# Kernel optimization log

Measured on AMD Instinct MI355X. Metric: run time of the kernel, lower is better.

Reference implementation:

```python
import jax, jax.numpy as jnp
import numpy as np

B, CIN, COUT, N, T, K = 16, 32, 64, 1024, 64, 3


def setup_inputs() -> dict:
    key = jax.random.key(0)
    k1, k2, k3 = jax.random.split(key, 3)
    x = jax.random.normal(k1, (B, CIN, N, T), dtype=jnp.float32)
    # scaled laplacian-like support (keep spectral radius ~1 so Chebyshev terms stay bounded)
    adj = jax.random.normal(k2, (N, N), dtype=jnp.float32) / np.sqrt(N).astype(np.float32)
    W = jax.random.normal(k3, (4 * COUT, (CIN + COUT) * K), dtype=jnp.float32) * 0.02
    b = jnp.zeros((4 * COUT,), dtype=jnp.float32)
    return {"x": x, "adj": adj, "W": W, "b": b}


def reference(x, adj, W, b):
    Bn, cin, Nn, Tn = x.shape
    c_out = W.shape[0] // 4
    feat_in = W.shape[1] // K  # = cin + c_out

    # Chebyshev polynomial basis of adj (loop-invariant across time; compute once)
    Ls = [jnp.eye(Nn, dtype=x.dtype), adj]
    for _ in range(2, K):
        Ls.append(2.0 * (adj @ Ls[-1]) - Ls[-2])
    Lap = jnp.stack(Ls, 0)  # [K, N, N]; Ls[k][q, n]

    # Conv1d(kernel=1) weight reshaped to match channel flatten order (c major, k minor)
    Wr = W.reshape(4 * c_out, feat_in, K)  # [4*c_out, F, K]
    bb = b[None, :, None]

    def step(carry, xt):
        h, c = carry
        tem = jnp.concatenate([xt, h], axis=1)  # [B, F, N]
        # einsum('bcn,knq->bckq', x, Lap.T) == einsum('bfn,kqn->bfkq', x, Lap)
        g = jnp.einsum('bfn,kqn->bfkq', tem, Lap)  # [B, F, K, N]
        fea = jnp.einsum('bfkq,ofk->boq', g, Wr) + bb  # [B, 4*c_out, N]
        i, j, f, o = jnp.split(fea, 4, axis=1)
        new_c = c * jax.nn.sigmoid(f) + jax.nn.sigmoid(i) * jnp.tanh(j)
        new_h = jnp.tanh(new_c) * jax.nn.sigmoid(o)
        return (new_h, new_c), new_h

    h0 = jnp.zeros((Bn, c_out, Nn), dtype=x.dtype)
    c0 = jnp.zeros((Bn, c_out, Nn), dtype=x.dtype)
    x_t = jnp.moveaxis(x, -1, 0)  # [T, B, cin, N]
    _, outs = jax.lax.scan(step, (h0, c0), x_t)  # [T, B, c_out, N]
    return jnp.moveaxis(outs, 0, -1)  # [B, c_out, N, T]
```

## Files before the change

kernel.cpp:

```cpp
#include <hip/hip_runtime.h>
#include <stdint.h>


#define Bb   16
#define CIN  32
#define COUT 64
#define Nn   1024
#define Tt   64
#define Ff   96
#define G4   256
#define KJ   288

#define BUFSZ 57344
#define GQLO  37888
#define GQP   592

typedef unsigned short u16;
typedef short short8 __attribute__((ext_vector_type(8)));
typedef short short4v __attribute__((ext_vector_type(4)));
typedef float f32x4 __attribute__((ext_vector_type(4)));

static __device__ __forceinline__ u16 f2bf(float f) {
    union { float f; uint32_t u; } v; v.f = f;
    uint32_t r = v.u + 0x7FFFu + ((v.u >> 16) & 1u);
    return (u16)(r >> 16);
}
static __device__ __forceinline__ float bf2f(u16 h) {
    union { uint32_t u; float f; } v; v.u = ((uint32_t)h) << 16;
    return v.f;
}
static __device__ __forceinline__ float sigm(float x) { return 1.0f / (1.0f + expf(-x)); }

static __device__ __forceinline__ void gload16(const void* g, void* l) {
    __builtin_amdgcn_global_load_lds(
        (const __attribute__((address_space(1))) void*)g,
        (__attribute__((address_space(3))) void*)l, 16, 0, 0);
}

__global__ void k_fill(float* out, int n, float v) {
    int i = blockIdx.x * 256 + threadIdx.x;
    if (i < n) out[i] = v;
}

__global__ __launch_bounds__(256) void k_adj_split(const float* __restrict__ adj,
                                                   u16* __restrict__ hi, u16* __restrict__ lo) {
    int i = blockIdx.x * 256 + threadIdx.x;
    float v = adj[i];
    u16 h = f2bf(v);
    hi[i] = h; lo[i] = f2bf(v - bf2f(h));
}

__global__ __launch_bounds__(256) void k_adj_t(const float* __restrict__ adj,
                                               u16* __restrict__ th, u16* __restrict__ tl_) {
    __shared__ float tile[64][65];
    int m0 = blockIdx.x * 64, n0 = blockIdx.y * 64;
    int tid = threadIdx.x;
    #pragma unroll
    for (int i = 0; i < 16; i++) {
        int lin = i * 256 + tid;
        int ml = lin >> 6, nl = lin & 63;
        tile[ml][nl] = adj[(size_t)(m0 + ml) * Nn + n0 + nl];
    }
    __syncthreads();
    #pragma unroll
    for (int i = 0; i < 16; i++) {
        int lin = i * 256 + tid;
        int nl = lin >> 6, ml = lin & 63;
        float v = tile[ml][nl];
        u16 h = f2bf(v);
        size_t off = (size_t)(n0 + nl) * Nn + m0 + ml;
        th[off] = h; tl_[off] = f2bf(v - bf2f(h));
    }
}

__global__ __launch_bounds__(256) void k_l2(
    const u16* __restrict__ a_hi, const u16* __restrict__ a_lo,
    const u16* __restrict__ bt_hi, const u16* __restrict__ bt_lo,
    u16* __restrict__ o_hi, u16* __restrict__ o_lo)
{
    __shared__ u16 Ah[64][40], Al[64][40], Bh[64][40], Bl[64][40];
    const int tid = threadIdx.x, lane = tid & 63, w = tid >> 6;
    const int wm = (w >> 1) * 32, wn = (w & 1) * 32;
    const int r0 = blockIdx.x * 64, q0 = blockIdx.y * 64;
    const int srow = tid >> 2, scol = (tid & 3) * 8;
    const u16* arh = a_hi + (size_t)(r0 + srow) * Nn;
    const u16* arl = a_lo + (size_t)(r0 + srow) * Nn;
    const u16* brh = bt_hi + (size_t)(q0 + srow) * Nn;
    const u16* brl = bt_lo + (size_t)(q0 + srow) * Nn;

    f32x4 acc[2][2];
    #pragma unroll
    for (int i = 0; i < 2; i++)
        #pragma unroll
        for (int j = 0; j < 2; j++) acc[i][j] = (f32x4){0.f, 0.f, 0.f, 0.f};

    for (int k0 = 0; k0 < Nn; k0 += 32) {
        __syncthreads();
        *(short8*)&Ah[srow][scol] = *(const short8*)&arh[k0 + scol];
        *(short8*)&Al[srow][scol] = *(const short8*)&arl[k0 + scol];
        *(short8*)&Bh[srow][scol] = *(const short8*)&brh[k0 + scol];
        *(short8*)&Bl[srow][scol] = *(const short8*)&brl[k0 + scol];
        __syncthreads();
        const int kb = (lane >> 4) * 8;
        short8 ah[2], al[2], bh[2], bl[2];
        #pragma unroll
        for (int mi = 0; mi < 2; mi++) {
            int row = wm + mi * 16 + (lane & 15);
            ah[mi] = *(const short8*)&Ah[row][kb];
            al[mi] = *(const short8*)&Al[row][kb];
        }
        #pragma unroll
        for (int ni = 0; ni < 2; ni++) {
            int col = wn + ni * 16 + (lane & 15);
            bh[ni] = *(const short8*)&Bh[col][kb];
            bl[ni] = *(const short8*)&Bl[col][kb];
        }
        #pragma unroll
        for (int mi = 0; mi < 2; mi++)
            #pragma unroll
            for (int ni = 0; ni < 2; ni++) {
                acc[mi][ni] = __builtin_amdgcn_mfma_f32_16x16x32_bf16(ah[mi], bh[ni], acc[mi][ni], 0, 0, 0);
                acc[mi][ni] = __builtin_amdgcn_mfma_f32_16x16x32_bf16(al[mi], bh[ni], acc[mi][ni], 0, 0, 0);
                acc[mi][ni] = __builtin_amdgcn_mfma_f32_16x16x32_bf16(ah[mi], bl[ni], acc[mi][ni], 0, 0, 0);
            }
    }
    #pragma unroll
    for (int mi = 0; mi < 2; mi++)
        #pragma unroll
        for (int ni = 0; ni < 2; ni++)
            #pragma unroll
            for (int j = 0; j < 4; j++) {
                int rr = r0 + wm + mi * 16 + (lane >> 4) * 4 + j;
                int qq = q0 + wn + ni * 16 + (lane & 15);
                float v = 2.f * acc[mi][ni][j] - ((rr == qq) ? 1.f : 0.f);
                size_t off = (size_t)rr * Nn + qq;
                u16 hh = f2bf(v);
                o_hi[off] = hh; o_lo[off] = f2bf(v - bf2f(hh));
            }
}

__global__ __launch_bounds__(256) void k_w_split(const float* __restrict__ W,
                                                 u16* __restrict__ hi, u16* __restrict__ lo) {
    int idx = blockIdx.x * 256 + threadIdx.x;
    int o = idx / KJ, j = idx - o * KJ;
    int k = j / Ff, f = j - k * Ff;
    float v = W[(size_t)o * KJ + f * 3 + k];
    u16 h = f2bf(v);
    hi[idx] = h; lo[idx] = f2bf(v - bf2f(h));
}

__global__ __launch_bounds__(256) void k_x_split(const float* __restrict__ x,
        u16* __restrict__ xf_hi, u16* __restrict__ xf_lo,
        u16* __restrict__ xq_hi, u16* __restrict__ xq_lo) {
    __shared__ float tile[64][65];
    int n0 = blockIdx.x * 64;
    int bc = blockIdx.y;
    const float* src = x + (size_t)bc * Nn * Tt;
    int tid = threadIdx.x;
    #pragma unroll
    for (int i = 0; i < 16; i++) {
        int lin = i * 256 + tid;
        int nl = lin >> 6, tl = lin & 63;
        tile[nl][tl] = src[(size_t)(n0 + nl) * Tt + tl];
    }
    __syncthreads();
    int b = bc >> 5, ch = bc & 31;
    #pragma unroll
    for (int i = 0; i < 16; i++) {
        int lin = i * 256 + tid;
        int tl = lin >> 6, nl = lin & 63;
        float v = tile[nl][tl];
        u16 h = f2bf(v), l = f2bf(v - bf2f(h));
        size_t off = (((size_t)tl * Bb + b) * CIN + ch) * Nn + n0 + nl;
        xf_hi[off] = h; xf_lo[off] = l;
        size_t off2 = (((size_t)tl * Bb + b) * Nn + n0 + nl) * CIN + ch;
        xq_hi[off2] = h; xq_lo[off2] = l;
    }
}

__global__ __launch_bounds__(512) void k_step(
    int t,
    const u16* __restrict__ xsf_hi, const u16* __restrict__ xsf_lo,
    const u16* __restrict__ xsq_hi, const u16* __restrict__ xsq_lo,
    u16* __restrict__ hf_hi, u16* __restrict__ hf_lo,
    u16* __restrict__ hq_hi, u16* __restrict__ hq_lo,
    const u16* __restrict__ bcat_hi, const u16* __restrict__ bcat_lo,
    const u16* __restrict__ Wh, const u16* __restrict__ Wl,
    const float* __restrict__ bias, float* __restrict__ cbuf,
    float* __restrict__ outbuf)
{
    __shared__ __attribute__((aligned(16))) char lds[114688];
    const int tid = threadIdx.x, lane = tid & 63, w = tid >> 6;
    const int q0 = blockIdx.x * 64;
    const int bb = blockIdx.y;

    const u16* srcb[7];
    #pragma unroll
    for (int i = 0; i < 7; i++) {
        int u = (i * 8 + w) * 64 + lane;
        if (u < 1536) {
            int hl = (u >= 768) ? 1 : 0;
            int r = (u - hl * 768) >> 3, c8 = u & 7;
            const u16* p;
            if (r < CIN) p = (hl ? xsf_lo : xsf_hi) + (size_t)((t * Bb + bb) * CIN + r) * Nn;
            else         p = (hl ? hf_lo  : hf_hi ) + (size_t)(bb * COUT + r - CIN) * Nn;
            srcb[i] = p + (c8 ^ (r & 7)) * 8;
        } else {
            int v = u - 1536;
            int hl = v >> 10;
            int r = (v & 1023) >> 3, c8 = v & 7;
            int grow = q0 + r + ((r >= 64) ? (Nn - 64) : 0);
            srcb[i] = (hl ? bcat_lo : bcat_hi) + (size_t)grow * Nn + (c8 ^ (r & 7)) * 8;
        }
    }

    const int wr = w >> 2, wc = w & 3;
    f32x4 acc[3][2];
    #pragma unroll
    for (int i = 0; i < 3; i++)
        #pragma unroll
        for (int j = 0; j < 2; j++) acc[i][j] = (f32x4){0.f, 0.f, 0.f, 0.f};

    #pragma unroll
    for (int i = 0; i < 7; i++)
        gload16(srcb[i], lds + (i * 8 + w) * 1024);

    for (int kc = 0; kc < 16; kc++) {
        if (kc < 15) {
            const int nb = ((kc + 1) & 1) * BUFSZ;
            const int k0 = (kc + 1) * 64;
            #pragma unroll
            for (int i = 0; i < 7; i++)
                gload16(srcb[i] + k0, lds + nb + (i * 8 + w) * 1024);
            asm volatile("s_waitcnt vmcnt(7)" ::: "memory");
        } else {
            asm volatile("s_waitcnt vmcnt(0)" ::: "memory");
        }
        __builtin_amdgcn_s_barrier();
        const char* bo = lds + (kc & 1) * BUFSZ;
        #pragma unroll
        for (int kk = 0; kk < 2; kk++) {
            const int ksw = kk * 4 + (lane >> 4);
            short8 ah[3], al[3], bh[2], bl[2];
            #pragma unroll
            for (int mi = 0; mi < 3; mi++) {
                int r = wr * 48 + mi * 16 + (lane & 15);
                int off = r * 128 + ((ksw ^ (r & 7)) << 4);
                ah[mi] = *(const short8*)(bo + off);
                al[mi] = *(const short8*)(bo + 12288 + off);
            }
            #pragma unroll
            for (int ni = 0; ni < 2; ni++) {
                int rb = wc * 32 + ni * 16 + (lane & 15);
                int off = 24576 + rb * 128 + ((ksw ^ (rb & 7)) << 4);
                bh[ni] = *(const short8*)(bo + off);
                bl[ni] = *(const short8*)(bo + 16384 + off);
            }
            #pragma unroll
            for (int mi = 0; mi < 3; mi++)
                #pragma unroll
                for (int ni = 0; ni < 2; ni++) {
                    acc[mi][ni] = __builtin_amdgcn_mfma_f32_16x16x32_bf16(ah[mi], bh[ni], acc[mi][ni], 0, 0, 0);
                    acc[mi][ni] = __builtin_amdgcn_mfma_f32_16x16x32_bf16(al[mi], bh[ni], acc[mi][ni], 0, 0, 0);
                    acc[mi][ni] = __builtin_amdgcn_mfma_f32_16x16x32_bf16(ah[mi], bl[ni], acc[mi][ni], 0, 0, 0);
                }
        }
        __builtin_amdgcn_s_barrier();
    }

    {
        int q = tid >> 3, j4 = (tid & 7) * 4;
        size_t sx = ((size_t)(t * Bb + bb) * Nn + q0 + q) * CIN + j4;
        *(short4v*)(lds + q * GQP + j4 * 2)        = *(const short4v*)&xsq_hi[sx];
        *(short4v*)(lds + GQLO + q * GQP + j4 * 2) = *(const short4v*)&xsq_lo[sx];
    }
    #pragma unroll
    for (int i = 0; i < 2; i++) {
        int u = i * 512 + tid;
        int q = u >> 4, j4 = (u & 15) * 4;
        size_t sh = ((size_t)bb * Nn + q0 + q) * COUT + j4;
        *(short4v*)(lds + q * GQP + (32 + j4) * 2)        = *(const short4v*)&hq_hi[sh];
        *(short4v*)(lds + GQLO + q * GQP + (32 + j4) * 2) = *(const short4v*)&hq_lo[sh];
    }
    #pragma unroll
    for (int mi = 0; mi < 3; mi++)
        #pragma unroll
        for (int ni = 0; ni < 2; ni++) {
            int col = wc * 32 + ni * 16 + (lane & 15);
            int g = col >> 6, ql = col & 63;
            int f0 = wr * 48 + mi * 16 + (lane >> 4) * 4;
            int jd = 96 + g * 96 + f0;
            short4v vh, vl;
            #pragma unroll
            for (int j = 0; j < 4; j++) {
                float v = acc[mi][ni][j];
                u16 hh = f2bf(v);
                vh[j] = (short)hh;
                vl[j] = (short)f2bf(v - bf2f(hh));
            }
            *(short4v*)(lds + ql * GQP + jd * 2) = vh;
            *(short4v*)(lds + GQLO + ql * GQP + jd * 2) = vl;
        }
    __syncthreads();

    f32x4 a2[2][4];
    #pragma unroll
    for (int i = 0; i < 2; i++)
        #pragma unroll
        for (int j = 0; j < 4; j++) a2[i][j] = (f32x4){0.f, 0.f, 0.f, 0.f};

    const int kb8 = (lane >> 4) * 8;
    #pragma unroll
    for (int c = 0; c < 9; c++) {
        int j0 = c * 32;
        short8 wh[2], wl2[2], gh[4], gl[4];
        #pragma unroll
        for (int mi = 0; mi < 2; mi++) {
            int o = w * 32 + mi * 16 + (lane & 15);
            size_t so = (size_t)o * KJ + j0 + kb8;
            wh[mi]  = *(const short8*)&Wh[so];
            wl2[mi] = *(const short8*)&Wl[so];
        }
        #pragma unroll
        for (int ni = 0; ni < 4; ni++) {
            int q = ni * 16 + (lane & 15);
            int off = q * GQP + (j0 + kb8) * 2;
            gh[ni] = *(const short8*)(lds + off);
            gl[ni] = *(const short8*)(lds + GQLO + off);
        }
        #pragma unroll
        for (int mi = 0; mi < 2; mi++)
            #pragma unroll
            for (int ni = 0; ni < 4; ni++) {
                a2[mi][ni] = __builtin_amdgcn_mfma_f32_16x16x32_bf16(wh[mi],  gh[ni], a2[mi][ni], 0, 0, 0);
                a2[mi][ni] = __builtin_amdgcn_mfma_f32_16x16x32_bf16(wl2[mi], gh[ni], a2[mi][ni], 0, 0, 0);
                a2[mi][ni] = __builtin_amdgcn_mfma_f32_16x16x32_bf16(wh[mi],  gl[ni], a2[mi][ni], 0, 0, 0);
            }
    }
    __syncthreads();

    #pragma unroll
    for (int mi = 0; mi < 2; mi++) {
        int o0 = w * 32 + mi * 16 + (lane >> 4) * 4;
        f32x4 bv = *(const f32x4*)&bias[o0];
        #pragma unroll
        for (int ni = 0; ni < 4; ni++) {
            int q = ni * 16 + (lane & 15);
            f32x4 v = a2[mi][ni] + bv;
            *(f32x4*)(lds + q * 1040 + o0 * 4) = v;
        }
    }
    __syncthreads();

    {
        const float* FEA = (const float*)lds;
        int q = tid & 63, qg = q0 + q;
        int co0 = (tid >> 6) * 8;
        const float* fr = FEA + q * 260;
        #pragma unroll
        for (int ii = 0; ii < 8; ii++) {
            int co = co0 + ii;
            float iv = fr[co];
            float jv = fr[co + 64];
            float fv = fr[co + 128];
            float ov = fr[co + 192];
            size_t cof = ((size_t)(bb * COUT + co)) * Nn + qg;
            float cc = cbuf[cof];
            float nc = cc * sigm(fv) + sigm(iv) * tanhf(jv);
            float nh = tanhf(nc) * sigm(ov);
            cbuf[cof] = nc;
            u16 hh = f2bf(nh), hl2 = f2bf(nh - bf2f(hh));
            hf_hi[cof] = hh; hf_lo[cof] = hl2;
            size_t hq = ((size_t)bb * Nn + qg) * COUT + co;
            hq_hi[hq] = hh; hq_lo[hq] = hl2;
            outbuf[((size_t)(t * Bb + bb) * COUT + co) * Nn + qg] = nh;
        }
    }
}

__global__ __launch_bounds__(256) void k_out_t(const float* __restrict__ outbuf,
                                               float* __restrict__ out) {
    __shared__ float tile[64][65];
    int q0 = blockIdx.x * 64;
    int bo = blockIdx.y;
    int b = bo >> 6, o = bo & 63;
    int tid = threadIdx.x;
    #pragma unroll
    for (int i = 0; i < 16; i++) {
        int lin = i * 256 + tid;
        int tl = lin >> 6, ql = lin & 63;
        tile[tl][ql] = outbuf[(((size_t)tl * Bb + b) * COUT + o) * Nn + q0 + ql];
    }
    __syncthreads();
    #pragma unroll
    for (int i = 0; i < 16; i++) {
        int lin = i * 256 + tid;
        int ql = lin >> 6, tl = lin & 63;
        out[((size_t)bo * Nn + q0 + ql) * Tt + tl] = tile[tl][ql];
    }
}

extern "C" void kernel_launch(void* const* d_in, const int* in_sizes, int n_in,
                              void* d_out, int out_size, void* d_ws, size_t ws_size,
                              hipStream_t stream)
{
    const float* x    = (const float*)d_in[0];
    const float* adj  = (const float*)d_in[1];
    const float* W    = (const float*)d_in[2];
    const float* bias = (const float*)d_in[3];
    float* out = (float*)d_out;

    size_t off = 0;
    char* base = (char*)d_ws;
    auto take = [&](size_t bytes) -> void* {
        void* r = base + off;
        off += (bytes + 255) & ~(size_t)255;
        return r;
    };
    u16* bcat_hi = (u16*)take(2ull * 2 * Nn * Nn);
    u16* bcat_lo = (u16*)take(2ull * 2 * Nn * Nn);
    u16* adjT_hi = (u16*)take(2ull * Nn * Nn);
    u16* adjT_lo = (u16*)take(2ull * Nn * Nn);
    u16* xsf_hi  = (u16*)take(2ull * Tt * Bb * CIN * Nn);
    u16* xsf_lo  = (u16*)take(2ull * Tt * Bb * CIN * Nn);
    u16* xsq_hi  = (u16*)take(2ull * Tt * Bb * CIN * Nn);
    u16* xsq_lo  = (u16*)take(2ull * Tt * Bb * CIN * Nn);
    u16* hf_hi   = (u16*)take(2ull * Bb * COUT * Nn);
    u16* hf_lo   = (u16*)take(2ull * Bb * COUT * Nn);
    u16* hq_hi   = (u16*)take(2ull * Bb * COUT * Nn);
    u16* hq_lo   = (u16*)take(2ull * Bb * COUT * Nn);
    float* cbuf  = (float*)take(4ull * Bb * COUT * Nn);
    u16* Wc_hi   = (u16*)take(2ull * G4 * KJ);
    u16* Wc_lo   = (u16*)take(2ull * G4 * KJ);
    float* outbuf = (float*)take(4ull * (size_t)Tt * Bb * COUT * Nn);

    if (off > ws_size) {
        float v = (float)(ws_size >> 20);
        k_fill<<<dim3((out_size + 255) / 256), 256, 0, stream>>>(out, out_size, v);
        return;
    }

    hipMemsetAsync(hf_hi, 0, 2ull * Bb * COUT * Nn, stream);
    hipMemsetAsync(hf_lo, 0, 2ull * Bb * COUT * Nn, stream);
    hipMemsetAsync(hq_hi, 0, 2ull * Bb * COUT * Nn, stream);
    hipMemsetAsync(hq_lo, 0, 2ull * Bb * COUT * Nn, stream);
    hipMemsetAsync(cbuf, 0, 4ull * Bb * COUT * Nn, stream);

    k_adj_split<<<dim3((Nn * Nn) / 256), 256, 0, stream>>>(adj, bcat_hi, bcat_lo);
    k_adj_t<<<dim3(16, 16), 256, 0, stream>>>(adj, adjT_hi, adjT_lo);
    k_l2<<<dim3(16, 16), 256, 0, stream>>>(bcat_hi, bcat_lo, adjT_hi, adjT_lo,
                                           bcat_hi + (size_t)Nn * Nn, bcat_lo + (size_t)Nn * Nn);
    k_w_split<<<dim3((G4 * KJ) / 256), 256, 0, stream>>>(W, Wc_hi, Wc_lo);
    k_x_split<<<dim3(Nn / 64, Bb * CIN), 256, 0, stream>>>(x, xsf_hi, xsf_lo, xsq_hi, xsq_lo);

    for (int t = 0; t < Tt; t++) {
        k_step<<<dim3(16, 16), 512, 0, stream>>>(t,
            xsf_hi, xsf_lo, xsq_hi, xsq_lo,
            hf_hi, hf_lo, hq_hi, hq_lo,
            bcat_hi, bcat_lo, Wc_hi, Wc_lo,
            bias, cbuf, outbuf);
    }
    k_out_t<<<dim3(Nn / 64, Bb * COUT), 256, 0, stream>>>(outbuf, out);
}
```

Before: 3.089 ms.

## Halve per-step tile width to double grid size and capture identity term from LDS

```diff
diff --git a/kernel.cpp b/kernel.cpp
--- a/kernel.cpp
+++ b/kernel.cpp
@@ -11,9 +11,9 @@
 #define G4   256
 #define KJ   288
 
-#define BUFSZ 57344
-#define GQLO  37888
-#define GQP   592
+#define BUFSZ 40960
+#define GQPB  624
+#define GQLO  19968
 
 typedef unsigned short u16;
 typedef short short8 __attribute__((ext_vector_type(8)));
@@ -150,8 +150,7 @@
 }
 
 __global__ __launch_bounds__(256) void k_x_split(const float* __restrict__ x,
-        u16* __restrict__ xf_hi, u16* __restrict__ xf_lo,
-        u16* __restrict__ xq_hi, u16* __restrict__ xq_lo) {
+        u16* __restrict__ xf_hi, u16* __restrict__ xf_lo) {
     __shared__ float tile[64][65];
     int n0 = blockIdx.x * 64;
     int bc = blockIdx.y;
@@ -173,31 +172,28 @@
         u16 h = f2bf(v), l = f2bf(v - bf2f(h));
         size_t off = (((size_t)tl * Bb + b) * CIN + ch) * Nn + n0 + nl;
         xf_hi[off] = h; xf_lo[off] = l;
-        size_t off2 = (((size_t)tl * Bb + b) * Nn + n0 + nl) * CIN + ch;
-        xq_hi[off2] = h; xq_lo[off2] = l;
-    }
-}
-
-__global__ __launch_bounds__(512) void k_step(
+    }
+}
+
+__global__ __launch_bounds__(512, 4) void k_step(
     int t,
     const u16* __restrict__ xsf_hi, const u16* __restrict__ xsf_lo,
-    const u16* __restrict__ xsq_hi, const u16* __restrict__ xsq_lo,
     u16* __restrict__ hf_hi, u16* __restrict__ hf_lo,
-    u16* __restrict__ hq_hi, u16* __restrict__ hq_lo,
     const u16* __restrict__ bcat_hi, const u16* __restrict__ bcat_lo,
     const u16* __restrict__ Wh, const u16* __restrict__ Wl,
     const float* __restrict__ bias, float* __restrict__ cbuf,
     float* __restrict__ outbuf)
 {
-    __shared__ __attribute__((aligned(16))) char lds[114688];
+    __shared__ __attribute__((aligned(16))) char lds[81920];
     const int tid = threadIdx.x, lane = tid & 63, w = tid >> 6;
-    const int q0 = blockIdx.x * 64;
+    const int bx = blockIdx.x;
+    const int q0g = bx * 32;
     const int bb = blockIdx.y;
 
-    const u16* srcb[7];
-    #pragma unroll
-    for (int i = 0; i < 7; i++) {
-        int u = (i * 8 + w) * 64 + lane;
+    const u16* srcb[5];
+    #pragma unroll
+    for (int i = 0; i < 5; i++) {
+        int u = i * 512 + tid;
         if (u < 1536) {
             int hl = (u >= 768) ? 1 : 0;
             int r = (u - hl * 768) >> 3, c8 = u & 7;
@@ -207,32 +203,35 @@
             srcb[i] = p + (c8 ^ (r & 7)) * 8;
         } else {
             int v = u - 1536;
-            int hl = v >> 10;
-            int r = (v & 1023) >> 3, c8 = v & 7;
-            int grow = q0 + r + ((r >= 64) ? (Nn - 64) : 0);
+            int hl = v >> 9;
+            int r = (v & 511) >> 3, c8 = v & 7;
+            int grow = q0g + (r & 31) + ((r >= 32) ? Nn : 0);
             srcb[i] = (hl ? bcat_lo : bcat_hi) + (size_t)grow * Nn + (c8 ^ (r & 7)) * 8;
         }
     }
 
     const int wr = w >> 2, wc = w & 3;
-    f32x4 acc[3][2];
-    #pragma unroll
-    for (int i = 0; i < 3; i++)
-        #pragma unroll
-        for (int j = 0; j < 2; j++) acc[i][j] = (f32x4){0.f, 0.f, 0.f, 0.f};
-
-    #pragma unroll
-    for (int i = 0; i < 7; i++)
-        gload16(srcb[i], lds + (i * 8 + w) * 1024);
+    f32x4 acc[3];
+    #pragma unroll
+    for (int i = 0; i < 3; i++) acc[i] = (f32x4){0.f, 0.f, 0.f, 0.f};
+
+    u16 cxh[6], cxl[6];
+    #pragma unroll
+    for (int i = 0; i < 6; i++) { cxh[i] = 0; cxl[i] = 0; }
+    const int capkc = bx >> 1;
+
+    #pragma unroll
+    for (int i = 0; i < 5; i++)
+        gload16(srcb[i], lds + (i * 512 + tid) * 16);
 
     for (int kc = 0; kc < 16; kc++) {
         if (kc < 15) {
-            const int nb = ((kc + 1) & 1) * BUFSZ;
+            char* nb = lds + ((kc + 1) & 1) * BUFSZ;
             const int k0 = (kc + 1) * 64;
             #pragma unroll
-            for (int i = 0; i < 7; i++)
-                gload16(srcb[i] + k0, lds + nb + (i * 8 + w) * 1024);
-            asm volatile("s_waitcnt vmcnt(7)" ::: "memory");
+            for (int i = 0; i < 5; i++)
+                gload16(srcb[i] + k0, nb + (i * 512 + tid) * 16);
+            asm volatile("s_waitcnt vmcnt(5)" ::: "memory");
         } else {
             asm volatile("s_waitcnt vmcnt(0)" ::: "memory");
         }
@@ -241,7 +240,7 @@
         #pragma unroll
         for (int kk = 0; kk < 2; kk++) {
             const int ksw = kk * 4 + (lane >> 4);
-            short8 ah[3], al[3], bh[2], bl[2];
+            short8 ah[3], al[3], bh, bl;
             #pragma unroll
             for (int mi = 0; mi < 3; mi++) {
                 int r = wr * 48 + mi * 16 + (lane & 15);
@@ -249,71 +248,77 @@
                 ah[mi] = *(const short8*)(bo + off);
                 al[mi] = *(const short8*)(bo + 12288 + off);
             }
-            #pragma unroll
-            for (int ni = 0; ni < 2; ni++) {
-                int rb = wc * 32 + ni * 16 + (lane & 15);
+            {
+                int rb = wc * 16 + (lane & 15);
                 int off = 24576 + rb * 128 + ((ksw ^ (rb & 7)) << 4);
-                bh[ni] = *(const short8*)(bo + off);
-                bl[ni] = *(const short8*)(bo + 16384 + off);
-            }
-            #pragma unroll
-            for (int mi = 0; mi < 3; mi++)
-                #pragma unroll
-                for (int ni = 0; ni < 2; ni++) {
-                    acc[mi][ni] = __builtin_amdgcn_mfma_f32_16x16x32_bf16(ah[mi], bh[ni], acc[mi][ni], 0, 0, 0);
-                    acc[mi][ni] = __builtin_amdgcn_mfma_f32_16x16x32_bf16(al[mi], bh[ni], acc[mi][ni], 0, 0, 0);
-                    acc[mi][ni] = __builtin_amdgcn_mfma_f32_16x16x32_bf16(ah[mi], bl[ni], acc[mi][ni], 0, 0, 0);
-                }
+                bh = *(const short8*)(bo + off);
+                bl = *(const short8*)(bo + 8192 + off);
+            }
+            #pragma unroll
+            for (int mi = 0; mi < 3; mi++) {
+                acc[mi] = __builtin_amdgcn_mfma_f32_16x16x32_bf16(ah[mi], bh, acc[mi], 0, 0, 0);
+                acc[mi] = __builtin_amdgcn_mfma_f32_16x16x32_bf16(al[mi], bh, acc[mi], 0, 0, 0);
+                acc[mi] = __builtin_amdgcn_mfma_f32_16x16x32_bf16(ah[mi], bl, acc[mi], 0, 0, 0);
+            }
+        }
+        if (kc == capkc) {
+            int q = lane & 31;
+            int jg = (w << 1) | (lane >> 5);
+            int lc = ((bx & 1) << 5) | q;
+            int u8 = lc >> 3, byoff = (lc & 7) * 2;
+            #pragma unroll
+            for (int jj = 0; jj < 6; jj++) {
+                int j = jg * 6 + jj;
+                int off = j * 128 + (((u8) ^ (j & 7)) << 4) + byoff;
+                cxh[jj] = *(const u16*)(bo + off);
+                cxl[jj] = *(const u16*)(bo + 12288 + off);
+            }
+            asm volatile("s_waitcnt lgkmcnt(0)" ::: "memory");
+            __builtin_amdgcn_sched_barrier(0);
         }
         __builtin_amdgcn_s_barrier();
     }
 
     {
-        int q = tid >> 3, j4 = (tid & 7) * 4;
-        size_t sx = ((size_t)(t * Bb + bb) * Nn + q0 + q) * CIN + j4;
-        *(short4v*)(lds + q * GQP + j4 * 2)        = *(const short4v*)&xsq_hi[sx];
-        *(short4v*)(lds + GQLO + q * GQP + j4 * 2) = *(const short4v*)&xsq_lo[sx];
-    }
-    #pragma unroll
-    for (int i = 0; i < 2; i++) {
-        int u = i * 512 + tid;
-        int q = u >> 4, j4 = (u & 15) * 4;
-        size_t sh = ((size_t)bb * Nn + q0 + q) * COUT + j4;
-        *(short4v*)(lds + q * GQP + (32 + j4) * 2)        = *(const short4v*)&hq_hi[sh];
-        *(short4v*)(lds + GQLO + q * GQP + (32 + j4) * 2) = *(const short4v*)&hq_lo[sh];
-    }
-    #pragma unroll
-    for (int mi = 0; mi < 3; mi++)
-        #pragma unroll
-        for (int ni = 0; ni < 2; ni++) {
-            int col = wc * 32 + ni * 16 + (lane & 15);
-            int g = col >> 6, ql = col & 63;
-            int f0 = wr * 48 + mi * 16 + (lane >> 4) * 4;
-            int jd = 96 + g * 96 + f0;
-            short4v vh, vl;
-            #pragma unroll
-            for (int j = 0; j < 4; j++) {
-                float v = acc[mi][ni][j];
-                u16 hh = f2bf(v);
-                vh[j] = (short)hh;
-                vl[j] = (short)f2bf(v - bf2f(hh));
-            }
-            *(short4v*)(lds + ql * GQP + jd * 2) = vh;
-            *(short4v*)(lds + GQLO + ql * GQP + jd * 2) = vl;
-        }
-    __syncthreads();
-
-    f32x4 a2[2][4];
+        int q = lane & 31;
+        int jg = (w << 1) | (lane >> 5);
+        #pragma unroll
+        for (int jj = 0; jj < 6; jj++) {
+            int j = jg * 6 + jj;
+            *(u16*)(lds + q * GQPB + j * 2) = cxh[jj];
+            *(u16*)(lds + GQLO + q * GQPB + j * 2) = cxl[jj];
+        }
+    }
+    #pragma unroll
+    for (int mi = 0; mi < 3; mi++) {
+        int c = wc * 16 + (lane & 15);
+        int g = c >> 5, ql = c & 31;
+        int f0 = wr * 48 + mi * 16 + (lane >> 4) * 4;
+        int jd = 96 + g * 96 + f0;
+        short4v vh, vl;
+        #pragma unroll
+        for (int j = 0; j < 4; j++) {
+            float v = acc[mi][j];
+            u16 hh = f2bf(v);
+            vh[j] = (short)hh;
+            vl[j] = (short)f2bf(v - bf2f(hh));
+        }
+        *(short4v*)(lds + ql * GQPB + jd * 2) = vh;
+        *(short4v*)(lds + GQLO + ql * GQPB + jd * 2) = vl;
+    }
+    __syncthreads();
+
+    f32x4 a2[2][2];
     #pragma unroll
     for (int i = 0; i < 2; i++)
         #pragma unroll
-        for (int j = 0; j < 4; j++) a2[i][j] = (f32x4){0.f, 0.f, 0.f, 0.f};
+        for (int j = 0; j < 2; j++) a2[i][j] = (f32x4){0.f, 0.f, 0.f, 0.f};
 
     const int kb8 = (lane >> 4) * 8;
     #pragma unroll
     for (int c = 0; c < 9; c++) {
         int j0 = c * 32;
-        short8 wh[2], wl2[2], gh[4], gl[4];
+        short8 wh[2], wl2[2], gh[2], gl[2];
         #pragma unroll
         for (int mi = 0; mi < 2; mi++) {
             int o = w * 32 + mi * 16 + (lane & 15);
@@ -322,16 +327,16 @@
             wl2[mi] = *(const short8*)&Wl[so];
         }
         #pragma unroll
-        for (int ni = 0; ni < 4; ni++) {
+        for (int ni = 0; ni < 2; ni++) {
             int q = ni * 16 + (lane & 15);
-            int off = q * GQP + (j0 + kb8) * 2;
+            int off = q * GQPB + (j0 + kb8) * 2;
             gh[ni] = *(const short8*)(lds + off);
             gl[ni] = *(const short8*)(lds + GQLO + off);
         }
         #pragma unroll
         for (int mi = 0; mi < 2; mi++)
             #pragma unroll
-            for (int ni = 0; ni < 4; ni++) {
+            for (int ni = 0; ni < 2; ni++) {
                 a2[mi][ni] = __builtin_amdgcn_mfma_f32_16x16x32_bf16(wh[mi],  gh[ni], a2[mi][ni], 0, 0, 0);
                 a2[mi][ni] = __builtin_amdgcn_mfma_f32_16x16x32_bf16(wl2[mi], gh[ni], a2[mi][ni], 0, 0, 0);
                 a2[mi][ni] = __builtin_amdgcn_mfma_f32_16x16x32_bf16(wh[mi],  gl[ni], a2[mi][ni], 0, 0, 0);
@@ -339,40 +344,41 @@
     }
     __syncthreads();
 
-    #pragma unroll
-    for (int mi = 0; mi < 2; mi++) {
-        int o0 = w * 32 + mi * 16 + (lane >> 4) * 4;
-        f32x4 bv = *(const f32x4*)&bias[o0];
-        #pragma unroll
-        for (int ni = 0; ni < 4; ni++) {
-            int q = ni * 16 + (lane & 15);
-            f32x4 v = a2[mi][ni] + bv;
-            *(f32x4*)(lds + q * 1040 + o0 * 4) = v;
-        }
-    }
-    __syncthreads();
-
     {
-        const float* FEA = (const float*)lds;
-        int q = tid & 63, qg = q0 + q;
-        int co0 = (tid >> 6) * 8;
-        const float* fr = FEA + q * 260;
-        #pragma unroll
-        for (int ii = 0; ii < 8; ii++) {
+        float* FEAf = (float*)lds;
+        #pragma unroll
+        for (int mi = 0; mi < 2; mi++) {
+            int o0 = w * 32 + mi * 16 + (lane >> 4) * 4;
+            f32x4 bv = *(const f32x4*)&bias[o0];
+            #pragma unroll
+            for (int ni = 0; ni < 2; ni++) {
+                int q = ni * 16 + (lane & 15);
+                #pragma unroll
+                for (int j = 0; j < 4; j++)
+                    FEAf[(o0 + j) * 33 + q] = a2[mi][ni][j] + bv[j];
+            }
+        }
+    }
+    __syncthreads();
+
+    {
+        const float* FEAf = (const float*)lds;
+        int q = tid & 31, qg = q0g + q;
+        int co0 = (tid >> 5) * 4;
+        #pragma unroll
+        for (int ii = 0; ii < 4; ii++) {
             int co = co0 + ii;
-            float iv = fr[co];
-            float jv = fr[co + 64];
-            float fv = fr[co + 128];
-            float ov = fr[co + 192];
+            float iv = FEAf[co * 33 + q];
+            float jv = FEAf[(co + 64) * 33 + q];
+            float fv = FEAf[(co + 128) * 33 + q];
+            float ov = FEAf[(co + 192) * 33 + q];
             size_t cof = ((size_t)(bb * COUT + co)) * Nn + qg;
             float cc = cbuf[cof];
             float nc = cc * sigm(fv) + sigm(iv) * tanhf(jv);
             float nh = tanhf(nc) * sigm(ov);
             cbuf[cof] = nc;
-            u16 hh = f2bf(nh), hl2 = f2bf(nh - bf2f(hh));
-            hf_hi[cof] = hh; hf_lo[cof] = hl2;
-            size_t hq = ((size_t)bb * Nn + qg) * COUT + co;
-            hq_hi[hq] = hh; hq_lo[hq] = hl2;
+            u16 hh = f2bf(nh);
+            hf_hi[cof] = hh; hf_lo[cof] = f2bf(nh - bf2f(hh));
             outbuf[((size_t)(t * Bb + bb) * COUT + co) * Nn + qg] = nh;
         }
     }
@@ -423,12 +429,8 @@
     u16* adjT_lo = (u16*)take(2ull * Nn * Nn);
     u16* xsf_hi  = (u16*)take(2ull * Tt * Bb * CIN * Nn);
     u16* xsf_lo  = (u16*)take(2ull * Tt * Bb * CIN * Nn);
-    u16* xsq_hi  = (u16*)take(2ull * Tt * Bb * CIN * Nn);
-    u16* xsq_lo  = (u16*)take(2ull * Tt * Bb * CIN * Nn);
     u16* hf_hi   = (u16*)take(2ull * Bb * COUT * Nn);
     u16* hf_lo   = (u16*)take(2ull * Bb * COUT * Nn);
-    u16* hq_hi   = (u16*)take(2ull * Bb * COUT * Nn);
-    u16* hq_lo   = (u16*)take(2ull * Bb * COUT * Nn);
     float* cbuf  = (float*)take(4ull * Bb * COUT * Nn);
     u16* Wc_hi   = (u16*)take(2ull * G4 * KJ);
     u16* Wc_lo   = (u16*)take(2ull * G4 * KJ);
@@ -442,8 +444,6 @@
 
     hipMemsetAsync(hf_hi, 0, 2ull * Bb * COUT * Nn, stream);
     hipMemsetAsync(hf_lo, 0, 2ull * Bb * COUT * Nn, stream);
-    hipMemsetAsync(hq_hi, 0, 2ull * Bb * COUT * Nn, stream);
-    hipMemsetAsync(hq_lo, 0, 2ull * Bb * COUT * Nn, stream);
     hipMemsetAsync(cbuf, 0, 4ull * Bb * COUT * Nn, stream);
 
     k_adj_split<<<dim3((Nn * Nn) / 256), 256, 0, stream>>>(adj, bcat_hi, bcat_lo);
@@ -451,12 +451,11 @@
     k_l2<<<dim3(16, 16), 256, 0, stream>>>(bcat_hi, bcat_lo, adjT_hi, adjT_lo,
                                            bcat_hi + (size_t)Nn * Nn, bcat_lo + (size_t)Nn * Nn);
     k_w_split<<<dim3((G4 * KJ) / 256), 256, 0, stream>>>(W, Wc_hi, Wc_lo);
-    k_x_split<<<dim3(Nn / 64, Bb * CIN), 256, 0, stream>>>(x, xsf_hi, xsf_lo, xsq_hi, xsq_lo);
+    k_x_split<<<dim3(Nn / 64, Bb * CIN), 256, 0, stream>>>(x, xsf_hi, xsf_lo);
 
     for (int t = 0; t < Tt; t++) {
-        k_step<<<dim3(16, 16), 512, 0, stream>>>(t,
-            xsf_hi, xsf_lo, xsq_hi, xsq_lo,
-            hf_hi, hf_lo, hq_hi, hq_lo,
+        k_step<<<dim3(32, 16), 512, 0, stream>>>(t,
+            xsf_hi, xsf_lo, hf_hi, hf_lo,
             bcat_hi, bcat_lo, Wc_hi, Wc_lo,
             bias, cbuf, outbuf);
     }
```

Measured after the change: 2.565 ms. -17.0%, faster.
